# Kernel optimization log

Hardware: AMD Instinct MI355X
Metric: run time of the kernel (lower is better)

## Reference

```python
import jax, jax.numpy as jnp
import numpy as np

H = 512  # hidden_dimension
B = 32
S = 2048


def setup_inputs() -> dict:
    key = jax.random.key(0)
    k1, k2, k3, k4, k5, k6 = jax.random.split(key, 6)
    decoder_hide = jax.random.normal(k1, (B, H), dtype=jnp.float32)
    encoder_out = jax.random.normal(k2, (B, S, 2 * H), dtype=jnp.float32)
    mask = jax.random.randint(k3, (B, S), 0, 2, dtype=jnp.int32)
    bound = 1.0 / np.sqrt(3 * H)
    W_attn = jax.random.uniform(k4, (3 * H, H), minval=-bound, maxval=bound, dtype=jnp.float32)
    b_attn = jax.random.uniform(k5, (H,), minval=-bound, maxval=bound, dtype=jnp.float32)
    bound_v = 1.0 / np.sqrt(H)
    v_w = jax.random.uniform(k6, (H,), minval=-bound_v, maxval=bound_v, dtype=jnp.float32)
    return {"decoder_hide": decoder_hide, "encoder_out": encoder_out, "mask": mask,
            "W_attn": W_attn, "b_attn": b_attn, "v_w": v_w}


def reference(decoder_hide, encoder_out, mask, W_attn, b_attn, v_w):
    # Split the concat-linear: cat((h, enc)) @ W == h @ W[:H] + enc @ W[H:]
    W_h = W_attn[:H]        # [H, H]
    W_e = W_attn[H:]        # [2H, H]
    dec_proj = decoder_hide @ W_h + b_attn                 # [B, H]
    enc_proj = jnp.einsum('bse,eh->bsh', encoder_out, W_e)  # [B, S, H]
    energy = jnp.tanh(enc_proj + dec_proj[:, None, :])      # [B, S, H]
    attention = jnp.einsum('bsh,h->bs', energy, v_w)        # [B, S]
    attention = jnp.where(mask == 0, jnp.float32(-100000.0), attention)
    return jax.nn.softmax(attention, axis=1)
```

## Files before the change

### kernel.cpp

```cpp
#include <hip/hip_runtime.h>
#include <hip/hip_bf16.h>
#include <math.h>

#define Hdim 512
#define Bdim 32
#define Sdim 2048
#define Kdim 1024
#define Mtot (Bdim * Sdim)

#define BM 128
#define BN 128
#define BK 64

typedef __attribute__((ext_vector_type(8))) short short8;
typedef __attribute__((ext_vector_type(4))) float floatx4;

__device__ __forceinline__ short f2bf(float f) {
    union { float f; unsigned u; } v; v.f = f;
    unsigned r = v.u + 0x7fffu + ((v.u >> 16) & 1u);
    return (short)(r >> 16);
}

__device__ __forceinline__ short8 cvt8(float4 a, float4 b) {
    union { short8 s; __hip_bfloat162 h[4]; } u;
    u.h[0] = __float22bfloat162_rn(make_float2(a.x, a.y));
    u.h[1] = __float22bfloat162_rn(make_float2(a.z, a.w));
    u.h[2] = __float22bfloat162_rn(make_float2(b.x, b.y));
    u.h[3] = __float22bfloat162_rn(make_float2(b.z, b.w));
    return u.s;
}

__device__ __forceinline__ float fast_tanh(float x) {
    float ax = fabsf(x);
    float e  = __expf(-2.0f * ax);
    float r  = (1.0f - e) / (1.0f + e);
    return copysignf(r, x);
}

__global__ __launch_bounds__(256) void prep_kernel(
    const float* __restrict__ W_attn, const float* __restrict__ dec,
    const float* __restrict__ b_attn, short* __restrict__ Wb,
    float* __restrict__ dec_proj)
{
    const int t = threadIdx.x;
    if (blockIdx.x < 512) {
        const float* We = W_attn + Hdim * Hdim;
        __shared__ short tile[32][33];
        const int k0 = (blockIdx.x >> 4) * 32;
        const int n0 = (blockIdx.x & 15) * 32;
        const int r = t >> 5, c = t & 31;
        #pragma unroll
        for (int rr = 0; rr < 4; ++rr)
            tile[r + rr * 8][c] = f2bf(We[(size_t)(k0 + r + rr * 8) * Hdim + n0 + c]);
        __syncthreads();
        #pragma unroll
        for (int rr = 0; rr < 4; ++rr)
            Wb[(size_t)(n0 + r + rr * 8) * Kdim + k0 + c] = tile[c][r + rr * 8];
    } else {
        __shared__ float partl[2][128];
        const int bid = blockIdx.x - 512;
        const int b  = bid >> 2;
        const int cb = bid & 3;
        const int c  = cb * 128 + (t & 127);
        const int kh = t >> 7;
        float acc = 0.0f;
        const int kbeg = kh * 256, kend = kbeg + 256;
        #pragma unroll 8
        for (int k = kbeg; k < kend; ++k)
            acc = fmaf(dec[b * Hdim + k], W_attn[(size_t)k * Hdim + c], acc);
        partl[kh][t & 127] = acc;
        __syncthreads();
        if (t < 128)
            dec_proj[b * Hdim + cb * 128 + t] = partl[0][t] + partl[1][t] + b_attn[cb * 128 + t];
    }
}

__global__ __launch_bounds__(256, 3) void scores_kernel(
    const float* __restrict__ enc,
    const short* __restrict__ Wb,
    const float* __restrict__ dec_proj,
    const float* __restrict__ v_w,
    float* __restrict__ part)
{
    __shared__ __align__(16) short Asm[BM * BK];
    __shared__ __align__(16) short Bsm[BN * BK];
    __shared__ float redl[BM][2];

    const int t    = threadIdx.x;
    const int nblk = blockIdx.x & 3;
    const int mblk = blockIdx.x >> 2;
    const int row0 = mblk * BM;
    const int n0   = nblk * BN;
    const int b    = row0 / Sdim;

    const int w    = t >> 6;
    const int lane = t & 63;
    const int ln   = lane & 15;
    const int quad = lane >> 4;
    const int wr   = (w >> 1) * 64;
    const int wc   = (w & 1) * 64;

    const int sm  = t >> 1;
    const int sh  = t & 1;
    const int smx = sm & 7;
    const float* Ag = enc + (size_t)(row0 + sm) * Kdim + sh * 32;
    short* Aw = Asm + sm * BK;
    int awc[4];
    #pragma unroll
    for (int i = 0; i < 4; ++i) awc[i] = ((sh * 4 + i) ^ smx) * 8;

    const int l3 = lane >> 3, l7 = lane & 7;
    int boff[4];
    #pragma unroll
    for (int r = 0; r < 4; ++r)
        boff[r] = (n0 + (w * 4 + r) * 8 + l3) * Kdim + ((l7 ^ l3) * 8);
    short* bbase = Bsm + w * 2048;

    const int lnx = ln & 7;
    int arow[4], brow[4];
    #pragma unroll
    for (int i = 0; i < 4; ++i) {
        arow[i] = (wr + i * 16 + ln) * BK;
        brow[i] = (wc + i * 16 + ln) * BK;
    }
    const int pf0 = ((0 * 4 + quad) ^ lnx) * 8;
    const int pf1 = ((1 * 4 + quad) ^ lnx) * 8;

    floatx4 acc[4][4];
    #pragma unroll
    for (int i = 0; i < 4; ++i)
        #pragma unroll
        for (int j = 0; j < 4; ++j)
            acc[i][j] = (floatx4)(0.0f);

    for (int kt = 0; kt < Kdim; kt += BK) {
        __syncthreads();
        #pragma unroll
        for (int r = 0; r < 4; ++r) {
            const short* gp = Wb + boff[r] + kt;
            __builtin_amdgcn_global_load_lds(
                (const __attribute__((address_space(1))) unsigned int*)(const void*)gp,
                (__attribute__((address_space(3))) unsigned int*)(void*)(bbase + r * 512),
                16, 0, 0);
        }
        {
            const float4* g = (const float4*)(Ag + kt);
            float4 f0 = g[0], f1 = g[1], f2 = g[2], f3 = g[3];
            float4 f4 = g[4], f5 = g[5], f6 = g[6], f7 = g[7];
            *(short8*)&Aw[awc[0]] = cvt8(f0, f1);
            *(short8*)&Aw[awc[1]] = cvt8(f2, f3);
            *(short8*)&Aw[awc[2]] = cvt8(f4, f5);
            *(short8*)&Aw[awc[3]] = cvt8(f6, f7);
        }
        __syncthreads();

        #pragma unroll
        for (int f = 0; f < 2; ++f) {
            const int pf = f ? pf1 : pf0;
            short8 af[4], bfr[4];
            #pragma unroll
            for (int i = 0; i < 4; ++i) af[i]  = *(const short8*)&Asm[arow[i] + pf];
            #pragma unroll
            for (int j = 0; j < 4; ++j) bfr[j] = *(const short8*)&Bsm[brow[j] + pf];
            #pragma unroll
            for (int i = 0; i < 4; ++i)
                #pragma unroll
                for (int j = 0; j < 4; ++j)
                    acc[i][j] = __builtin_amdgcn_mfma_f32_16x16x32_bf16(
                                    af[i], bfr[j], acc[i][j], 0, 0, 0);
        }
    }

    float dpv[4], vwv[4];
    #pragma unroll
    for (int j = 0; j < 4; ++j) {
        int col = n0 + wc + j * 16 + ln;
        dpv[j] = dec_proj[b * Hdim + col];
        vwv[j] = v_w[col];
    }
    #pragma unroll
    for (int i = 0; i < 4; ++i) {
        #pragma unroll
        for (int reg = 0; reg < 4; ++reg) {
            float s = 0.0f;
            #pragma unroll
            for (int j = 0; j < 4; ++j) {
                float x = acc[i][j][reg] + dpv[j];
                s = fmaf(vwv[j], fast_tanh(x), s);
            }
            s += __shfl_xor(s, 1, 64);
            s += __shfl_xor(s, 2, 64);
            s += __shfl_xor(s, 4, 64);
            s += __shfl_xor(s, 8, 64);
            if (ln == 0)
                redl[wr + i * 16 + quad * 4 + reg][w & 1] = s;
        }
    }
    __syncthreads();
    if (t < BM)
        part[(size_t)nblk * Mtot + row0 + t] = redl[t][0] + redl[t][1];
}

__global__ __launch_bounds__(256) void softmax_kernel(
    const float* __restrict__ part, const int* __restrict__ mask,
    float* __restrict__ out)
{
    __shared__ float sred[8];
    const int b = blockIdx.x;
    const int t = threadIdx.x;
    const int lane = t & 63;
    const int wid  = t >> 6;

    float x[8];
    float m = -1e30f;
    #pragma unroll
    for (int j = 0; j < 8; ++j) {
        int idx = b * Sdim + j * 256 + t;
        float v = part[idx] + part[Mtot + idx] + part[2 * Mtot + idx] + part[3 * Mtot + idx];
        if (mask[idx] == 0) v = -100000.0f;
        x[j] = v;
        m = fmaxf(m, v);
    }
    #pragma unroll
    for (int off = 32; off >= 1; off >>= 1)
        m = fmaxf(m, __shfl_xor(m, off, 64));
    if (lane == 0) sred[wid] = m;
    __syncthreads();
    m = fmaxf(fmaxf(sred[0], sred[1]), fmaxf(sred[2], sred[3]));

    float s = 0.0f;
    #pragma unroll
    for (int j = 0; j < 8; ++j) {
        float e = __expf(x[j] - m);
        x[j] = e;
        s += e;
    }
    #pragma unroll
    for (int off = 32; off >= 1; off >>= 1)
        s += __shfl_xor(s, off, 64);
    if (lane == 0) sred[4 + wid] = s;
    __syncthreads();
    s = sred[4] + sred[5] + sred[6] + sred[7];

    const float inv = 1.0f / s;
    #pragma unroll
    for (int j = 0; j < 8; ++j)
        out[b * Sdim + j * 256 + t] = x[j] * inv;
}

extern "C" void kernel_launch(void* const* d_in, const int* in_sizes, int n_in,
                              void* d_out, int out_size, void* d_ws, size_t ws_size,
                              hipStream_t stream) {
    const float* dec  = (const float*)d_in[0];
    const float* enc  = (const float*)d_in[1];
    const int*   mask = (const int*)  d_in[2];
    const float* W    = (const float*)d_in[3];
    const float* ba   = (const float*)d_in[4];
    const float* vw   = (const float*)d_in[5];
    float* out = (float*)d_out;

    float* dec_proj = (float*)d_ws;
    short* Wb       = (short*)(dec_proj + Bdim * Hdim);
    float* part     = (float*)(Wb + Hdim * Kdim);

    prep_kernel<<<640, 256, 0, stream>>>(W, dec, ba, Wb, dec_proj);
    scores_kernel<<<(Mtot / BM) * 4, 256, 0, stream>>>(enc, Wb, dec_proj, vw, part);
    softmax_kernel<<<Bdim, 256, 0, stream>>>(part, mask, out);
}
```

Baseline: 489.0 us.

## Cover full hidden width per block so encoder rows are read once

Changes the scores GEMM tiling from 128x128 tiles with four N-blocks per row group to 64-row tiles spanning all 512 output columns. Each encoder row is then loaded and converted to bf16 once instead of four times, and the cross-block partial-score buffer disappears, so softmax reads a single score. The per-thread accumulator doubles (32 MFMA tiles), LDS for B grows to 64 KB, and occupancy drops to 2 blocks per CU. Also swaps the tanh division for a hardware reciprocal.

```diff
diff --git a/kernel.cpp b/kernel.cpp
--- a/kernel.cpp
+++ b/kernel.cpp
@@ -8,8 +8,8 @@
 #define Kdim 1024
 #define Mtot (Bdim * Sdim)
 
-#define BM 128
-#define BN 128
+#define BM 64
+#define BN 512
 #define BK 64
 
 typedef __attribute__((ext_vector_type(8))) short short8;
@@ -33,7 +33,7 @@
 __device__ __forceinline__ float fast_tanh(float x) {
     float ax = fabsf(x);
     float e  = __expf(-2.0f * ax);
-    float r  = (1.0f - e) / (1.0f + e);
+    float r  = (1.0f - e) * __builtin_amdgcn_rcpf(1.0f + e);
     return copysignf(r, x);
 }
 
@@ -75,106 +75,91 @@
     }
 }
 
-__global__ __launch_bounds__(256, 3) void scores_kernel(
+__global__ __launch_bounds__(256, 2) void scores_kernel(
     const float* __restrict__ enc,
     const short* __restrict__ Wb,
     const float* __restrict__ dec_proj,
     const float* __restrict__ v_w,
-    float* __restrict__ part)
+    float* __restrict__ scores)
 {
     __shared__ __align__(16) short Asm[BM * BK];
     __shared__ __align__(16) short Bsm[BN * BK];
-    __shared__ float redl[BM][2];
+    __shared__ float redl[BM][4];
 
     const int t    = threadIdx.x;
-    const int nblk = blockIdx.x & 3;
-    const int mblk = blockIdx.x >> 2;
-    const int row0 = mblk * BM;
-    const int n0   = nblk * BN;
+    const int row0 = blockIdx.x * BM;
     const int b    = row0 / Sdim;
 
     const int w    = t >> 6;
     const int lane = t & 63;
     const int ln   = lane & 15;
     const int quad = lane >> 4;
-    const int wr   = (w >> 1) * 64;
-    const int wc   = (w & 1) * 64;
-
-    const int sm  = t >> 1;
-    const int sh  = t & 1;
-    const int smx = sm & 7;
-    const float* Ag = enc + (size_t)(row0 + sm) * Kdim + sh * 32;
+
+    const int sm = t >> 2;
+    const int sq = t & 3;
+    const float* Ag = enc + (size_t)(row0 + sm) * Kdim + sq * 16;
     short* Aw = Asm + sm * BK;
-    int awc[4];
-    #pragma unroll
-    for (int i = 0; i < 4; ++i) awc[i] = ((sh * 4 + i) ^ smx) * 8;
+    const int aw0 = ((2 * sq)     ^ (sm & 7)) * 8;
+    const int aw1 = ((2 * sq + 1) ^ (sm & 7)) * 8;
 
     const int l3 = lane >> 3, l7 = lane & 7;
-    int boff[4];
-    #pragma unroll
-    for (int r = 0; r < 4; ++r)
-        boff[r] = (n0 + (w * 4 + r) * 8 + l3) * Kdim + ((l7 ^ l3) * 8);
-    short* bbase = Bsm + w * 2048;
-
-    const int lnx = ln & 7;
-    int arow[4], brow[4];
-    #pragma unroll
-    for (int i = 0; i < 4; ++i) {
-        arow[i] = (wr + i * 16 + ln) * BK;
-        brow[i] = (wc + i * 16 + ln) * BK;
-    }
-    const int pf0 = ((0 * 4 + quad) ^ lnx) * 8;
-    const int pf1 = ((1 * 4 + quad) ^ lnx) * 8;
-
-    floatx4 acc[4][4];
+    const short* Bg0 = Wb + (size_t)(w * 128 + l3) * Kdim + ((l7 ^ l3) * 8);
+
+    int arow[4], brow[8];
+    #pragma unroll
+    for (int i = 0; i < 4; ++i) arow[i] = (i * 16 + ln) * BK;
+    #pragma unroll
+    for (int j = 0; j < 8; ++j) brow[j] = (w * 128 + j * 16 + ln) * BK;
+    const int pf0 = (quad       ^ (ln & 7)) * 8;
+    const int pf1 = ((4 + quad) ^ (ln & 7)) * 8;
+
+    floatx4 acc[4][8];
     #pragma unroll
     for (int i = 0; i < 4; ++i)
         #pragma unroll
-        for (int j = 0; j < 4; ++j)
+        for (int j = 0; j < 8; ++j)
             acc[i][j] = (floatx4)(0.0f);
 
     for (int kt = 0; kt < Kdim; kt += BK) {
         __syncthreads();
         #pragma unroll
-        for (int r = 0; r < 4; ++r) {
-            const short* gp = Wb + boff[r] + kt;
+        for (int r = 0; r < 16; ++r) {
             __builtin_amdgcn_global_load_lds(
-                (const __attribute__((address_space(1))) unsigned int*)(const void*)gp,
-                (__attribute__((address_space(3))) unsigned int*)(void*)(bbase + r * 512),
+                (const __attribute__((address_space(1))) unsigned int*)(const void*)
+                    (Bg0 + (size_t)r * 8 * Kdim + kt),
+                (__attribute__((address_space(3))) unsigned int*)(void*)
+                    (Bsm + (w * 128 + r * 8) * BK),
                 16, 0, 0);
         }
         {
             const float4* g = (const float4*)(Ag + kt);
             float4 f0 = g[0], f1 = g[1], f2 = g[2], f3 = g[3];
-            float4 f4 = g[4], f5 = g[5], f6 = g[6], f7 = g[7];
-            *(short8*)&Aw[awc[0]] = cvt8(f0, f1);
-            *(short8*)&Aw[awc[1]] = cvt8(f2, f3);
-            *(short8*)&Aw[awc[2]] = cvt8(f4, f5);
-            *(short8*)&Aw[awc[3]] = cvt8(f6, f7);
+            *(short8*)&Aw[aw0] = cvt8(f0, f1);
+            *(short8*)&Aw[aw1] = cvt8(f2, f3);
         }
         __syncthreads();
 
         #pragma unroll
         for (int f = 0; f < 2; ++f) {
             const int pf = f ? pf1 : pf0;
-            short8 af[4], bfr[4];
+            short8 af[4], bfr[8];
             #pragma unroll
             for (int i = 0; i < 4; ++i) af[i]  = *(const short8*)&Asm[arow[i] + pf];
             #pragma unroll
-            for (int j = 0; j < 4; ++j) bfr[j] = *(const short8*)&Bsm[brow[j] + pf];
+            for (int j = 0; j < 8; ++j) bfr[j] = *(const short8*)&Bsm[brow[j] + pf];
             #pragma unroll
             for (int i = 0; i < 4; ++i)
                 #pragma unroll
-                for (int j = 0; j < 4; ++j)
+                for (int j = 0; j < 8; ++j)
                     acc[i][j] = __builtin_amdgcn_mfma_f32_16x16x32_bf16(
                                     af[i], bfr[j], acc[i][j], 0, 0, 0);
         }
     }
 
-    float dpv[4], vwv[4];
-    #pragma unroll
-    for (int j = 0; j < 4; ++j) {
-        int col = n0 + wc + j * 16 + ln;
+    float dpv[8], vwv[8];
+    #pragma unroll
+    for (int j = 0; j < 8; ++j) {
+        int col = w * 128 + j * 16 + ln;
         dpv[j] = dec_proj[b * Hdim + col];
         vwv[j] = v_w[col];
     }
@@ -184,7 +169,7 @@
         for (int reg = 0; reg < 4; ++reg) {
             float s = 0.0f;
             #pragma unroll
-            for (int j = 0; j < 4; ++j) {
+            for (int j = 0; j < 8; ++j) {
                 float x = acc[i][j][reg] + dpv[j];
                 s = fmaf(vwv[j], fast_tanh(x), s);
             }
@@ -193,16 +178,16 @@
             s += __shfl_xor(s, 4, 64);
             s += __shfl_xor(s, 8, 64);
             if (ln == 0)
-                redl[wr + i * 16 + quad * 4 + reg][w & 1] = s;
+                redl[i * 16 + quad * 4 + reg][w] = s;
         }
     }
     __syncthreads();
     if (t < BM)
-        part[(size_t)nblk * Mtot + row0 + t] = redl[t][0] + redl[t][1];
+        scores[row0 + t] = redl[t][0] + redl[t][1] + redl[t][2] + redl[t][3];
 }
 
 __global__ __launch_bounds__(256) void softmax_kernel(
-    const float* __restrict__ part, const int* __restrict__ mask,
+    const float* __restrict__ scores, const int* __restrict__ mask,
     float* __restrict__ out)
 {
     __shared__ float sred[8];
@@ -216,7 +201,7 @@
     #pragma unroll
     for (int j = 0; j < 8; ++j) {
         int idx = b * Sdim + j * 256 + t;
-        float v = part[idx] + part[Mtot + idx] + part[2 * Mtot + idx] + part[3 * Mtot + idx];
+        float v = scores[idx];
         if (mask[idx] == 0) v = -100000.0f;
         x[j] = v;
         m = fmaxf(m, v);
@@ -261,9 +246,9 @@
 
     float* dec_proj = (float*)d_ws;
     short* Wb       = (short*)(dec_proj + Bdim * Hdim);
-    float* part     = (float*)(Wb + Hdim * Kdim);
+    float* scores   = (float*)(Wb + Hdim * Kdim);
 
     prep_kernel<<<640, 256, 0, stream>>>(W, dec, ba, Wb, dec_proj);
-    scores_kernel<<<(Mtot / BM) * 4, 256, 0, stream>>>(enc, Wb, dec_proj, vw, part);
-    softmax_kernel<<<Bdim, 256, 0, stream>>>(part, mask, out);
-}
+    scores_kernel<<<Mtot / BM, 256, 0, stream>>>(enc, Wb, dec_proj, vw, scores);
+    softmax_kernel<<<Bdim, 256, 0, stream>>>(scores, mask, out);
+}
```

Result: faster. 429.9 us (-12.1%).
